# Kernel tuning notes

Measured on AMD Instinct MI355X. Metric: run time of the kernel, lower is better.

## Reference

```python
import jax, jax.numpy as jnp
import numpy as np
from jax import lax

N, C, RC, H, W = 2, 256, 32, 64, 64  # RC = C // 8


def conv1x1(x, w, b):
    # x: [n,c,h,w], w: [o,c], b: [o]
    return jnp.einsum('nchw,oc->nohw', x, w) + b[None, :, None, None]


def conv3x3(x, w, b):
    # x: [n,c,h,w], w: [o,i,3,3]
    y = lax.conv_general_dilated(x, w, window_strides=(1, 1), padding='SAME',
                                 dimension_numbers=('NCHW', 'OIHW', 'NCHW'))
    return y + b[None, :, None, None]


def setup_inputs() -> dict:
    key = jax.random.key(0)
    ks = jax.random.split(key, 16)
    p = lambda k, s: jax.random.normal(k, s, dtype=jnp.float32) * 0.02
    z = lambda o: jnp.zeros((o,), jnp.float32)
    return {
        'rgb_feat': jax.random.normal(ks[0], (N, C, H, W), jnp.float32),
        'chm_feat': jax.random.normal(ks[1], (N, C, H, W), jnp.float32),
        'rgb_q_w': p(ks[2], (RC, C)), 'rgb_q_b': z(RC),
        'rgb_k_w': p(ks[3], (RC, C)), 'rgb_k_b': z(RC),
        'rgb_v_w': p(ks[4], (C, C)), 'rgb_v_b': z(C),
        'depth_q_w': p(ks[5], (RC, C)), 'depth_q_b': z(RC),
        'depth_k_w': p(ks[6], (RC, C)), 'depth_k_b': z(RC),
        'depth_v_w': p(ks[7], (C, C)), 'depth_v_b': z(C),
        'gate_w': p(ks[8], (C, 2 * C)), 'gate_b': z(C),
        'fus1_w': p(ks[9], (2 * C, 2 * C)), 'fus1_b': z(2 * C),
        'fus2_w': p(ks[10], (2 * C, 2 * C, 3, 3)), 'fus2_b': z(2 * C),
        'fus3_w': p(ks[11], (C, 2 * C)), 'fus3_b': z(C),
        'skip_w': p(ks[12], (C, 2 * C)), 'skip_b': z(C),
    }


def reference(rgb_feat, chm_feat,
              rgb_q_w, rgb_q_b, rgb_k_w, rgb_k_b, rgb_v_w, rgb_v_b,
              depth_q_w, depth_q_b, depth_k_w, depth_k_b, depth_v_w, depth_v_b,
              gate_w, gate_b, fus1_w, fus1_b, fus2_w, fus2_b,
              fus3_w, fus3_b, skip_w, skip_b):
    n, c, h, w = rgb_feat.shape
    hw = h * w
    flat = lambda t: t.reshape(n, t.shape[1], hw)

    rq = flat(conv1x1(rgb_feat, rgb_q_w, rgb_q_b))       # [n,rc,hw]
    rk = flat(conv1x1(rgb_feat, rgb_k_w, rgb_k_b))       # [n,rc,hw]
    rv = flat(conv1x1(rgb_feat, rgb_v_w, rgb_v_b))       # [n,c,hw]
    dq = flat(conv1x1(chm_feat, depth_q_w, depth_q_b))   # [n,rc,hw]
    dk = flat(conv1x1(chm_feat, depth_k_w, depth_k_b))   # [n,rc,hw]
    dv = flat(conv1x1(chm_feat, depth_v_w, depth_v_b))   # [n,c,hw]

    # rgb branch attended with depth-derived attention
    rgb_attn = jax.nn.softmax(jnp.einsum('nri,nrj->nij', dq, dk), axis=-1)  # [n,hw,hw]
    br = jnp.einsum('nci,nij->ncj', rv, rgb_attn).reshape(rgb_feat.shape) + rgb_feat

    # depth branch attended with rgb-derived attention
    depth_attn = jax.nn.softmax(jnp.einsum('nri,nrj->nij', rq, rk), axis=-1)
    bd = jnp.einsum('nci,nij->ncj', dv, depth_attn).reshape(chm_feat.shape) + chm_feat

    cat = jnp.concatenate([br, bd], axis=1)              # [n,2c,h,w]
    g = jax.nn.sigmoid(conv1x1(cat, gate_w, gate_b))     # [n,c,h,w]
    c_fused = br * g + bd * (1.0 - g)
    d_fused = br * bd
    f = jnp.concatenate([c_fused, d_fused], axis=1)      # [n,2c,h,w]

    y = jax.nn.relu(conv1x1(f, fus1_w, fus1_b))
    y = jax.nn.relu(conv3x3(y, fus2_w, fus2_b))
    y = conv1x1(y, fus3_w, fus3_b)
    fused = y + conv1x1(f, skip_w, skip_b)
    return fused
```

## Files before the change

### kernel.cpp

```cpp
#include <hip/hip_runtime.h>
#include <stdint.h>


typedef __bf16 bf16_t;
typedef __bf16 bf16x8 __attribute__((ext_vector_type(8)));
typedef float f32x4 __attribute__((ext_vector_type(4)));

#define HW 4096
#define NB 2

__device__ inline f32x4 mfma_bf16(bf16x8 a, bf16x8 b, f32x4 c) {
    return __builtin_amdgcn_mfma_f32_16x16x32_bf16(a, b, c, 0, 0, 0);
}

#define LBAR()                                                                 \
    do {                                                                       \
        asm volatile("s_waitcnt lgkmcnt(0)" ::: "memory");                     \
        __builtin_amdgcn_s_barrier();                                          \
        __builtin_amdgcn_sched_barrier(0);                                     \
    } while (0)

#define MAXJOB 12
struct CvtJobs {
    const float* src[MAXJOB];
    bf16_t* dst[MAXJOB];
    int vend[MAXJOB];
    int rowlen[MAXJOB];
    int rowstride[MAXJOB];
    int rowoff[MAXJOB];
};

__global__ __launch_bounds__(256) void prep_k(CvtJobs J, int totalvec, int cvtBlocks,
                                              const float* __restrict__ fus2_src,
                                              bf16_t* __restrict__ fus2_dst,
                                              const float* qr, const float* kr,
                                              const float* qd, const float* kd,
                                              const float* sb, const float* fb,
                                              float* BQK_R, float* BQK_D, float* BSUM) {
    const int b = blockIdx.x, t = threadIdx.x;
    if (b < cvtBlocks) {
        int gv = b * 256 + t;
        if (gv >= totalvec) return;
        int j = 0;
        while (gv >= J.vend[j]) j++;
        int vbase = (j == 0) ? 0 : J.vend[j - 1];
        int e = (gv - vbase) * 8;
        const float* s = J.src[j] + e;
        float4 f0 = *(const float4*)s;
        float4 f1 = *(const float4*)(s + 4);
        bf16x8 o;
        o[0] = (bf16_t)f0.x; o[1] = (bf16_t)f0.y; o[2] = (bf16_t)f0.z; o[3] = (bf16_t)f0.w;
        o[4] = (bf16_t)f1.x; o[5] = (bf16_t)f1.y; o[6] = (bf16_t)f1.z; o[7] = (bf16_t)f1.w;
        int di = e;
        if (J.rowlen[j])
            di = (e / J.rowlen[j]) * J.rowstride[j] + J.rowoff[j] + (e % J.rowlen[j]);
        *(bf16x8*)(J.dst[j] + di) = o;
    } else if (b < cvtBlocks + 9216) {
        int idx = (b - cvtBlocks) * 256 + t;
        int o = idx / 4608;
        int tt = idx % 4608;
        int t9 = tt / 512;
        int c  = tt % 512;
        fus2_dst[idx] = (bf16_t)fus2_src[(size_t)o * 4608 + c * 9 + t9];
    } else {
        if (t < 32) {
            BQK_R[t] = qr[t]; BQK_R[32 + t] = kr[t];
            BQK_D[t] = qd[t]; BQK_D[32 + t] = kd[t];
        }
        BSUM[t] = sb[t] + fb[t];
    }
}

__global__ __launch_bounds__(512) void proj_k(const bf16_t* __restrict__ WV_R,
                                              const bf16_t* __restrict__ WV_D,
                                              const bf16_t* __restrict__ WQK_R,
                                              const bf16_t* __restrict__ WQK_D,
                                              const bf16_t* __restrict__ XB,
                                              const float* __restrict__ vb_r,
                                              const float* __restrict__ vb_d,
                                              const float* __restrict__ bqk_r,
                                              const float* __restrict__ bqk_d,
                                              bf16_t* __restrict__ V4,
                                              bf16_t* __restrict__ QKT) {
    __shared__ bf16_t Bt[2][64][72];
    const int t = threadIdx.x, b = blockIdx.x;
    const int w = t >> 6, lane = t & 63, quad = lane >> 4, l16 = lane & 15;

    f32x4 zero = {0.f, 0.f, 0.f, 0.f};
    f32x4 acc[4] = {zero, zero, zero, zero};

    if (b < 512) {
        const int mb = b & 1, jb = (b >> 1) & 63, n = b >> 7;
        const bf16_t* Au = (n >= 2) ? WV_D : WV_R;
        const float* biasu = (n >= 2) ? vb_d : vb_r;
        const bf16_t* Bb = XB + (size_t)n * (256 * HW) + jb * 64;
        const bf16_t* Arow = Au + (size_t)(mb * 128 + w * 16 + l16) * 256 + quad * 8;

        bf16x8 v0 = *(const bf16x8*)(Bb + (size_t)lane * HW + w * 8);
        for (int k0 = 0; k0 < 256; k0 += 64) {
            LBAR();
#pragma unroll
            for (int e = 0; e < 8; e++) Bt[0][w * 8 + e][lane] = v0[e];
            LBAR();
            const int kn = (k0 + 64 < 256) ? k0 + 64 : 0;
            bf16x8 vp = *(const bf16x8*)(Bb + (size_t)(kn + lane) * HW + w * 8);
            bf16x8 a0 = *(const bf16x8*)(Arow + k0);
            bf16x8 a1 = *(const bf16x8*)(Arow + k0 + 32);
#pragma unroll
            for (int ns = 0; ns < 4; ns++) {
                bf16x8 b0 = *(const bf16x8*)&Bt[0][ns * 16 + l16][quad * 8];
                bf16x8 b1 = *(const bf16x8*)&Bt[0][ns * 16 + l16][32 + quad * 8];
                acc[ns] = mfma_bf16(a0, b0, acc[ns]);
                acc[ns] = mfma_bf16(a1, b1, acc[ns]);
            }
            v0 = vp;
        }
#pragma unroll
        for (int ns = 0; ns < 4; ns++) {
#pragma unroll
            for (int rr = 0; rr < 4; rr++) {
                int m = mb * 128 + w * 16 + quad * 4 + rr;
                int col = jb * 64 + ns * 16 + l16;
                V4[(size_t)n * 256 * HW + (size_t)m * HW + col] =
                    (bf16_t)(acc[ns][rr] + biasu[m]);
            }
        }
    } else {
        const int qb = b - 512;
        const int n2 = qb >> 5, jpair = qb & 31;
        const int g = w >> 2, wg = w & 3;
        const int jb = jpair * 2 + g;
        const bf16_t* Au = (n2 >= 2) ? WQK_D : WQK_R;
        const float* biasu = (n2 >= 2) ? bqk_d : bqk_r;
        const bf16_t* Bb = XB + (size_t)n2 * (256 * HW) + jb * 64;
        const bf16_t* Arow = Au + (size_t)(wg * 16 + l16) * 256 + quad * 8;

        bf16x8 v0 = *(const bf16x8*)(Bb + (size_t)lane * HW + wg * 16);
        bf16x8 v1 = *(const bf16x8*)(Bb + (size_t)lane * HW + wg * 16 + 8);
        for (int k0 = 0; k0 < 256; k0 += 64) {
            LBAR();
#pragma unroll
            for (int e = 0; e < 8; e++) Bt[g][wg * 16 + e][lane] = v0[e];
#pragma unroll
            for (int e = 0; e < 8; e++) Bt[g][wg * 16 + 8 + e][lane] = v1[e];
            LBAR();
            const int kn = (k0 + 64 < 256) ? k0 + 64 : 0;
            bf16x8 p0 = *(const bf16x8*)(Bb + (size_t)(kn + lane) * HW + wg * 16);
            bf16x8 p1 = *(const bf16x8*)(Bb + (size_t)(kn + lane) * HW + wg * 16 + 8);
            bf16x8 a0 = *(const bf16x8*)(Arow + k0);
            bf16x8 a1 = *(const bf16x8*)(Arow + k0 + 32);
#pragma unroll
            for (int ns = 0; ns < 4; ns++) {
                bf16x8 b0 = *(const bf16x8*)&Bt[g][ns * 16 + l16][quad * 8];
                bf16x8 b1 = *(const bf16x8*)&Bt[g][ns * 16 + l16][32 + quad * 8];
                acc[ns] = mfma_bf16(a0, b0, acc[ns]);
                acc[ns] = mfma_bf16(a1, b1, acc[ns]);
            }
            v0 = p0; v1 = p1;
        }
        const float scl = (wg < 2) ? 1.44269504f : 1.0f;
#pragma unroll
        for (int ns = 0; ns < 4; ns++) {
            int col = jb * 64 + ns * 16 + l16;
            union { bf16_t h[4]; unsigned long long u; } pk;
#pragma unroll
            for (int rr = 0; rr < 4; rr++) {
                int m = wg * 16 + quad * 4 + rr;
                pk.h[rr] = (bf16_t)((acc[ns][rr] + biasu[m]) * scl);
            }
            *(unsigned long long*)(QKT +
                ((size_t)n2 * HW + col) * 64 + wg * 16 + quad * 4) = pk.u;
        }
    }
}

template <int EPI, bool OUT_BF16>
__global__ __launch_bounds__(512) void gemm_k(const bf16_t* __restrict__ A,
                                              const bf16_t* __restrict__ A2,
                                              const bf16_t* __restrict__ B,
                                              const float* __restrict__ bias,
                                              const float* __restrict__ bias2,
                                              void* __restrict__ outp,
                                              const void* __restrict__ aux,
                                              int M, int K, size_t strideB, size_t strideO) {
    __shared__ bf16_t Bt[64][72];
    const int t = threadIdx.x;
    const int mb = blockIdx.x, jb = blockIdx.y, n = blockIdx.z;
    const int w = t >> 6, lane = t & 63, quad = lane >> 4, l16 = lane & 15;

    const bf16_t* Au = (n >= 2) ? A2 : A;
    const float* biasu = (n >= 2) ? bias2 : bias;

    const bf16_t* Bb = B + (size_t)n * strideB + jb * 64;

    f32x4 zero = {0.f, 0.f, 0.f, 0.f};
    f32x4 acc[4] = {zero, zero, zero, zero};

    const bf16_t* Arow = Au + (size_t)(mb * 128 + w * 16 + l16) * K + quad * 8;

    bf16x8 v0 = *(const bf16x8*)(Bb + (size_t)lane * HW + w * 8);
    for (int k0 = 0; k0 < K; k0 += 64) {
        LBAR();
#pragma unroll
        for (int e = 0; e < 8; e++) Bt[w * 8 + e][lane] = v0[e];
        LBAR();
        const int kn = (k0 + 64 < K) ? k0 + 64 : 0;
        bf16x8 vp = *(const bf16x8*)(Bb + (size_t)(kn + lane) * HW + w * 8);
        bf16x8 a0 = *(const bf16x8*)(Arow + k0);
        bf16x8 a1 = *(const bf16x8*)(Arow + k0 + 32);
#pragma unroll
        for (int ns = 0; ns < 4; ns++) {
            bf16x8 b0 = *(const bf16x8*)&Bt[ns * 16 + l16][quad * 8];
            bf16x8 b1 = *(const bf16x8*)&Bt[ns * 16 + l16][32 + quad * 8];
            acc[ns] = mfma_bf16(a0, b0, acc[ns]);
            acc[ns] = mfma_bf16(a1, b1, acc[ns]);
        }
        v0 = vp;
    }

    if (EPI == 7) {
        const int m_base = mb * 128 + w * 16 + quad * 4;
#pragma unroll
        for (int ns = 0; ns < 4; ns++) {
            int col = jb * 64 + ns * 16 + l16;
            union { bf16_t h[4]; unsigned long long u; } pk;
#pragma unroll
            for (int rr = 0; rr < 4; rr++) {
                float v = acc[ns][rr] + biasu[m_base + rr];
                pk.h[rr] = (bf16_t)(v > 0.f ? v : 0.f);
            }
            *(unsigned long long*)((bf16_t*)outp +
                ((size_t)n * HW + col) * 512 + m_base) = pk.u;
        }
    } else if (EPI == 5) {
        const bf16_t* catp = (const bf16_t*)aux;
        bf16_t* f = (bf16_t*)outp;
#pragma unroll
        for (int ns = 0; ns < 4; ns++) {
#pragma unroll
            for (int rr = 0; rr < 4; rr++) {
                int m = mb * 128 + w * 16 + quad * 4 + rr;
                int col = jb * 64 + ns * 16 + l16;
                float v = acc[ns][rr] + biasu[m];
                float g = 1.f / (1.f + __expf(-v));
                size_t base = (size_t)n * 512 * HW + (size_t)m * HW + col;
                float br = (float)catp[base];
                float bd = (float)catp[base + (size_t)256 * HW];
                size_t ob = (size_t)n * 1024 * HW + (size_t)m * HW + col;
                f[ob] = (bf16_t)(br * g + bd * (1.f - g));
                f[ob + (size_t)256 * HW] = (bf16_t)(br * bd);
            }
        }
    } else {
#pragma unroll
        for (int ns = 0; ns < 4; ns++) {
#pragma unroll
            for (int rr = 0; rr < 4; rr++) {
                int m = mb * 128 + w * 16 + quad * 4 + rr;
                int col = jb * 64 + ns * 16 + l16;
                float v = acc[ns][rr] + biasu[m];
                size_t oi = (size_t)n * strideO + (size_t)m * HW + col;
                if (OUT_BF16) ((bf16_t*)outp)[oi] = (bf16_t)v;
                else ((float*)outp)[oi] = v;
            }
        }
    }
}

__global__ __launch_bounds__(256) void conv3_k(const bf16_t* __restrict__ A,
                                               const bf16_t* __restrict__ Y1n,
                                               const float* __restrict__ bias,
                                               bf16_t* __restrict__ outp,
                                               size_t strideN) {
    __shared__ bf16_t kTn[198][72];
    const int t = threadIdx.x;
    const int lin = blockIdx.x;
    const int n = lin & 1, mb = (lin >> 1) & 3, y = lin >> 3;
    const int w = t >> 6, lane = t & 63, quad = lane >> 4, l16 = lane & 15;

    f32x4 zero = {0.f, 0.f, 0.f, 0.f};
    f32x4 acc[2][4];
#pragma unroll
    for (int i = 0; i < 2; i++)
#pragma unroll
        for (int j = 0; j < 4; j++) acc[i][j] = zero;

    const bf16_t* Yb = Y1n + (size_t)n * HW * 512;

    const bf16_t* Arow0 = A + (size_t)(mb * 128 + w * 32 + l16) * 4608 + quad * 8;
    const bf16_t* Arow1 = Arow0 + (size_t)16 * 4608;

    int pxs[7], seg[7], gidx[7];
    bool ok[7], act[7];
#pragma unroll
    for (int i = 0; i < 7; i++) {
        int slot = t + i * 256;
        act[i] = slot < 1584;
        int ps = act[i] ? (slot >> 3) : 0;
        pxs[i] = ps;
        seg[i] = slot & 7;
        int r = ps / 66, xm = ps % 66;
        int yy = y + r - 1, xx = xm - 1;
        ok[i] = act[i] && ((unsigned)yy < 64u) && ((unsigned)xx < 64u);
        gidx[i] = ok[i] ? (yy * 64 + xx) : 0;
    }

    bf16x8 vals[7];
#pragma unroll
    for (int i = 0; i < 7; i++) {
        bf16x8 v;
        if (ok[i]) {
            v = *(const bf16x8*)(Yb + (size_t)gidx[i] * 512 + seg[i] * 8);
        } else {
#pragma unroll
            for (int e = 0; e < 8; e++) v[e] = (bf16_t)0.f;
        }
        vals[i] = v;
    }

    for (int c0 = 0; c0 < 512; c0 += 64) {
        LBAR();
#pragma unroll
        for (int i = 0; i < 7; i++)
            if (act[i]) *(bf16x8*)&kTn[pxs[i]][seg[i] * 8] = vals[i];
        LBAR();

        const int cn = (c0 + 64) & 511;
#pragma unroll
        for (int i = 0; i < 7; i++) {
            bf16x8 v;
            if (ok[i]) {
                v = *(const bf16x8*)(Yb + (size_t)gidx[i] * 512 + cn + seg[i] * 8);
            } else {
#pragma unroll
                for (int e = 0; e < 8; e++) v[e] = (bf16_t)0.f;
            }
            vals[i] = v;
        }

#pragma unroll
        for (int t9 = 0; t9 < 9; t9++) {
            const int dy = t9 / 3, dx = t9 % 3;
            const bf16_t* ap0 = Arow0 + t9 * 512 + c0;
            const bf16_t* ap1 = Arow1 + t9 * 512 + c0;
            bf16x8 a00 = *(const bf16x8*)(ap0);
            bf16x8 a01 = *(const bf16x8*)(ap0 + 32);
            bf16x8 a10 = *(const bf16x8*)(ap1);
            bf16x8 a11 = *(const bf16x8*)(ap1 + 32);
#pragma unroll
            for (int ns = 0; ns < 4; ns++) {
                int p = dy * 66 + ns * 16 + l16 + dx;
                bf16x8 b0 = *(const bf16x8*)&kTn[p][quad * 8];
                bf16x8 b1 = *(const bf16x8*)&kTn[p][32 + quad * 8];
                acc[0][ns] = mfma_bf16(a00, b0, acc[0][ns]);
                acc[0][ns] = mfma_bf16(a01, b1, acc[0][ns]);
                acc[1][ns] = mfma_bf16(a10, b0, acc[1][ns]);
                acc[1][ns] = mfma_bf16(a11, b1, acc[1][ns]);
            }
        }
    }

#pragma unroll
    for (int ms = 0; ms < 2; ms++) {
#pragma unroll
        for (int ns = 0; ns < 4; ns++) {
#pragma unroll
            for (int rr = 0; rr < 4; rr++) {
                int m = mb * 128 + w * 32 + ms * 16 + quad * 4 + rr;
                int x = ns * 16 + l16;
                float v = acc[ms][ns][rr] + bias[m];
                v = v > 0.f ? v : 0.f;
                outp[(size_t)n * strideN + (size_t)m * HW + y * 64 + x] = (bf16_t)v;
            }
        }
    }
}

#define ASTEP(P, ASC, AVC, ASN, AVN, ITN)                                      \
    {                                                                          \
        _Pragma("unroll")                                                      \
        for (int ns = 0; ns < 4; ns++) {                                       \
            f32x4 s = mfma_bf16(ASC, bS[ns], zero);                            \
            union { bf16_t h[4]; unsigned long long u; } pk;                   \
            float zs = 0.f;                                                    \
            _Pragma("unroll")                                                  \
            for (int rr = 0; rr < 4; rr++) {                                   \
                pk.h[rr] = (bf16_t)__builtin_amdgcn_exp2f(s[rr]);              \
                zs += (float)pk.h[rr];                                         \
            }                                                                  \
            zacc[ns] += zs;                                                    \
            *(unsigned long long*)&PT[P][ns * 16 + l16][w * 16 + quad * 4] = pk.u; \
        }                                                                      \
        ASN = *(const bf16x8*)(Qa + (size_t)((ITN) & 63) * (64 * 64));         \
        AVN[0][0] = *(const bf16x8*)(Vr0 + ((ITN) & 63) * 64);                 \
        AVN[0][1] = *(const bf16x8*)(Vr0 + ((ITN) & 63) * 64 + 32);            \
        AVN[1][0] = *(const bf16x8*)(Vr1 + ((ITN) & 63) * 64);                 \
        AVN[1][1] = *(const bf16x8*)(Vr1 + ((ITN) & 63) * 64 + 32);            \
        asm volatile("s_waitcnt lgkmcnt(0)" ::: "memory");                     \
        __builtin_amdgcn_s_barrier();                                          \
        __builtin_amdgcn_sched_barrier(0);                                     \
        __builtin_amdgcn_s_setprio(1);                                         \
        _Pragma("unroll")                                                      \
        for (int ns = 0; ns < 4; ns++) {                                       \
            bf16x8 b0 = *(const bf16x8*)&PT[P][ns * 16 + l16][quad * 8];       \
            bf16x8 b1 = *(const bf16x8*)&PT[P][ns * 16 + l16][32 + quad * 8];  \
            _Pragma("unroll")                                                  \
            for (int ct = 0; ct < 2; ct++) {                                   \
                acc[ct][ns] = mfma_bf16(AVC[ct][0], b0, acc[ct][ns]);          \
                acc[ct][ns] = mfma_bf16(AVC[ct][1], b1, acc[ct][ns]);          \
            }                                                                  \
        }                                                                      \
        __builtin_amdgcn_s_setprio(0);                                         \
    }

__global__ __launch_bounds__(256) void attn3_k(const bf16_t* __restrict__ QKT,
                                               const bf16_t* __restrict__ V,
                                               const float* __restrict__ rgb_feat,
                                               const float* __restrict__ chm_feat,
                                               bf16_t* __restrict__ CAT) {
    __shared__ bf16_t PT[2][64][72];
    __shared__ float Zp[4][64];
    const int t = threadIdx.x;
    const int lin = blockIdx.x;
    const int cb = lin & 1, z = (lin >> 1) & 3, jb = lin >> 3;
    const int w = t >> 6, lane = t & 63, quad = lane >> 4, l16 = lane & 15;
    const int qs = z ^ 2, n = z & 1;

    const bf16_t* Q = QKT + (size_t)qs * HW * 64;

    bf16x8 bS[4];
#pragma unroll
    for (int ns = 0; ns < 4; ns++)
        bS[ns] = *(const bf16x8*)(Q + (size_t)(jb * 64 + ns * 16 + l16) * 64 + 32 + quad * 8);

    f32x4 zero = {0.f, 0.f, 0.f, 0.f};
    f32x4 acc[2][4];
#pragma unroll
    for (int i = 0; i < 2; i++)
#pragma unroll
        for (int j = 0; j < 4; j++) acc[i][j] = zero;
    float zacc[4] = {0.f, 0.f, 0.f, 0.f};

    const bf16_t* Vr0 = V + ((size_t)z * 256 + cb * 128 + w * 16 + l16) * HW + quad * 8;
    const bf16_t* Vr1 = Vr0 + (size_t)64 * HW;
    const bf16_t* Qa = Q + (size_t)(w * 16 + l16) * 64 + quad * 8;

    bf16x8 aSa, aSb, aVa[2][2], aVb[2][2];
    aSa = *(const bf16x8*)Qa;
    aVa[0][0] = *(const bf16x8*)(Vr0);
    aVa[0][1] = *(const bf16x8*)(Vr0 + 32);
    aVa[1][0] = *(const bf16x8*)(Vr1);
    aVa[1][1] = *(const bf16x8*)(Vr1 + 32);

    for (int ii = 0; ii < 32; ii++) {
        ASTEP(0, aSa, aVa, aSb, aVb, 2 * ii + 1);
        ASTEP(1, aSb, aVb, aSa, aVa, 2 * ii + 2);
    }

#pragma unroll
    for (int ns = 0; ns < 4; ns++) {
        zacc[ns] += __shfl_xor(zacc[ns], 16, 64);
        zacc[ns] += __shfl_xor(zacc[ns], 32, 64);
    }
    if (lane < 16) {
#pragma unroll
        for (int ns = 0; ns < 4; ns++) Zp[w][ns * 16 + lane] = zacc[ns];
    }
    __syncthreads();
    float rz[4];
#pragma unroll
    for (int ns = 0; ns < 4; ns++) {
        float ssum = 0.f;
#pragma unroll
        for (int ww = 0; ww < 4; ww++) ssum += Zp[ww][ns * 16 + l16];
        rz[ns] = 1.f / ssum;
    }

    const float* feat = ((z < 2) ? rgb_feat : chm_feat) + (size_t)n * 256 * HW;
    bf16_t* outp = CAT + (size_t)n * 512 * HW + (size_t)(z < 2 ? 0 : 256) * HW;
#pragma unroll
    for (int ct = 0; ct < 2; ct++) {
#pragma unroll
        for (int ns = 0; ns < 4; ns++) {
#pragma unroll
            for (int rr = 0; rr < 4; rr++) {
                int c = cb * 128 + ct * 64 + w * 16 + quad * 4 + rr;
                int col = jb * 64 + ns * 16 + l16;
                float v = acc[ct][ns][rr] * rz[ns] + feat[(size_t)c * HW + col];
                outp[(size_t)c * HW + col] = (bf16_t)v;
            }
        }
    }
}

extern "C" void kernel_launch(void* const* d_in, const int* in_sizes, int n_in,
                              void* d_out, int out_size, void* d_ws, size_t ws_size,
                              hipStream_t stream) {
    (void)in_sizes; (void)n_in; (void)out_size; (void)ws_size;

    const float* rgb_feat  = (const float*)d_in[0];
    const float* chm_feat  = (const float*)d_in[1];
    const float* rgb_q_w   = (const float*)d_in[2];
    const float* rgb_q_b   = (const float*)d_in[3];
    const float* rgb_k_w   = (const float*)d_in[4];
    const float* rgb_k_b   = (const float*)d_in[5];
    const float* rgb_v_w   = (const float*)d_in[6];
    const float* rgb_v_b   = (const float*)d_in[7];
    const float* depth_q_w = (const float*)d_in[8];
    const float* depth_q_b = (const float*)d_in[9];
    const float* depth_k_w = (const float*)d_in[10];
    const float* depth_k_b = (const float*)d_in[11];
    const float* depth_v_w = (const float*)d_in[12];
    const float* depth_v_b = (const float*)d_in[13];
    const float* gate_w    = (const float*)d_in[14];
    const float* gate_b    = (const float*)d_in[15];
    const float* fus1_w    = (const float*)d_in[16];
    const float* fus1_b    = (const float*)d_in[17];
    const float* fus2_w    = (const float*)d_in[18];
    const float* fus2_b    = (const float*)d_in[19];
    const float* fus3_w    = (const float*)d_in[20];
    const float* fus3_b    = (const float*)d_in[21];
    const float* skip_w    = (const float*)d_in[22];
    const float* skip_b    = (const float*)d_in[23];

    char* ws = (char*)d_ws;
    size_t off = 0;
    auto alloc = [&](size_t bytes) -> char* {
        char* p = ws + off;
        off += (bytes + 255) & ~(size_t)255;
        return p;
    };

    bf16_t* WQK_R = (bf16_t*)alloc(64 * 256 * 2);
    bf16_t* WQK_D = (bf16_t*)alloc(64 * 256 * 2);
    bf16_t* WV_R  = (bf16_t*)alloc(256 * 256 * 2);
    bf16_t* WV_D  = (bf16_t*)alloc(256 * 256 * 2);
    bf16_t* WGATE = (bf16_t*)alloc(256 * 512 * 2);
    bf16_t* WFUS1 = (bf16_t*)alloc(512 * 512 * 2);
    bf16_t* WFUS2 = (bf16_t*)alloc(512 * 4608 * 2);
    bf16_t* WCAT  = (bf16_t*)alloc(256 * 1024 * 2);
    float*  BQK_R = (float*)alloc(64 * 4);
    float*  BQK_D = (float*)alloc(64 * 4);
    float*  BSUM  = (float*)alloc(256 * 4);
    bf16_t* XB    = (bf16_t*)alloc((size_t)4 * 256 * HW * 2);
    bf16_t* QKT   = (bf16_t*)alloc((size_t)4 * HW * 64 * 2);
    bf16_t* V4    = (bf16_t*)alloc((size_t)4 * 256 * HW * 2);
    bf16_t* CAT   = (bf16_t*)alloc((size_t)NB * 512 * HW * 2);
    bf16_t* FY    = (bf16_t*)alloc((size_t)NB * 1024 * HW * 2);
    bf16_t* Y1    = (bf16_t*)alloc((size_t)NB * HW * 512 * 2);

    bf16_t* XR = XB;
    bf16_t* XC = XB + (size_t)2 * 256 * HW;

    CvtJobs J;
    int cum = 0, nj = 0;
    auto addjob = [&](const float* s, bf16_t* d, int cnt, int rl, int rs, int ro) {
        J.src[nj] = s; J.dst[nj] = d; cum += cnt / 8; J.vend[nj] = cum;
        J.rowlen[nj] = rl; J.rowstride[nj] = rs; J.rowoff[nj] = ro; nj++;
    };
    addjob(rgb_feat, XR, NB * 256 * HW, 0, 0, 0);
    addjob(chm_feat, XC, NB * 256 * HW, 0, 0, 0);
    addjob(rgb_q_w, WQK_R, 32 * 256, 0, 0, 0);
    addjob(rgb_k_w, WQK_R + 32 * 256, 32 * 256, 0, 0, 0);
    addjob(depth_q_w, WQK_D, 32 * 256, 0, 0, 0);
    addjob(depth_k_w, WQK_D + 32 * 256, 32 * 256, 0, 0, 0);
    addjob(rgb_v_w, WV_R, 256 * 256, 0, 0, 0);
    addjob(depth_v_w, WV_D, 256 * 256, 0, 0, 0);
    addjob(gate_w, WGATE, 256 * 512, 0, 0, 0);
    addjob(fus1_w, WFUS1, 512 * 512, 0, 0, 0);
    addjob(skip_w, WCAT, 256 * 512, 512, 1024, 0);
    addjob(fus3_w, WCAT, 256 * 512, 512, 1024, 512);
    int totalvec = cum;
    int cvtBlocks = (totalvec + 255) / 256;
    int prepBlocks = cvtBlocks + 9216 + 1;
    prep_k<<<dim3(prepBlocks), 256, 0, stream>>>(
        J, totalvec, cvtBlocks, fus2_w, WFUS2,
        rgb_q_b, rgb_k_b, depth_q_b, depth_k_b, skip_b, fus3_b,
        BQK_R, BQK_D, BSUM);

    proj_k<<<dim3(640), 512, 0, stream>>>(
        WV_R, WV_D, WQK_R, WQK_D, XB, rgb_v_b, depth_v_b, BQK_R, BQK_D, V4, QKT);

    attn3_k<<<dim3(512), 256, 0, stream>>>(QKT, V4, rgb_feat, chm_feat, CAT);

    gemm_k<5, true><<<dim3(2, 64, NB), 512, 0, stream>>>(
        WGATE, WGATE, CAT, gate_b, gate_b, FY, CAT, 256, 512, (size_t)512 * HW, 0);

    gemm_k<7, true><<<dim3(4, 64, NB), 512, 0, stream>>>(
        WFUS1, WFUS1, FY, fus1_b, fus1_b, Y1, nullptr, 512, 512, (size_t)1024 * HW, 0);

    conv3_k<<<dim3(512), 256, 0, stream>>>(WFUS2, Y1, fus2_b,
                                           FY + (size_t)512 * HW, (size_t)1024 * HW);

    gemm_k<0, false><<<dim3(2, 64, NB), 512, 0, stream>>>(
        WCAT, WCAT, FY, BSUM, BSUM, d_out, nullptr, 256, 1024, (size_t)1024 * HW, (size_t)256 * HW);
}
```

Measured before the change: 335.6 us.

## Warp-specialize attention into producer softmax and consumer PV waves

Splits the attention kernel into 4 producer waves that compute exp scores into shared memory and 4 consumer waves that run the P·V MFMAs, synchronized by alternating barriers on a double-buffered PT tile. Each block now covers all 256 channels for one column tile, so the score computation is no longer repeated across two channel-half blocks. Grid halves and block size doubles to 512 threads. This adds register pressure (16 accumulators per consumer wave) and tight barrier coupling between the two roles.

```diff
diff --git a/kernel.cpp b/kernel.cpp
--- a/kernel.cpp
+++ b/kernel.cpp
@@ -376,7 +376,7 @@
     }
 }
 
-#define ASTEP(P, ASC, AVC, ASN, AVN, ITN)                                      \
+#define PSTEP(P, ASC, ASN, ITN)                                                \
     {                                                                          \
         _Pragma("unroll")                                                      \
         for (int ns = 0; ns < 4; ns++) {                                       \
@@ -392,11 +392,13 @@
             *(unsigned long long*)&PT[P][ns * 16 + l16][w * 16 + quad * 4] = pk.u; \
         }                                                                      \
         ASN = *(const bf16x8*)(Qa + (size_t)((ITN) & 63) * (64 * 64));         \
-        AVN[0][0] = *(const bf16x8*)(Vr0 + ((ITN) & 63) * 64);                 \
-        AVN[0][1] = *(const bf16x8*)(Vr0 + ((ITN) & 63) * 64 + 32);            \
-        AVN[1][0] = *(const bf16x8*)(Vr1 + ((ITN) & 63) * 64);                 \
-        AVN[1][1] = *(const bf16x8*)(Vr1 + ((ITN) & 63) * 64 + 32);            \
         asm volatile("s_waitcnt lgkmcnt(0)" ::: "memory");                     \
+        __builtin_amdgcn_s_barrier();                                          \
+        __builtin_amdgcn_sched_barrier(0);                                     \
+    }
+
+#define CSTEP(P, AVC, AVN, ITN)                                                \
+    {                                                                          \
         __builtin_amdgcn_s_barrier();                                          \
         __builtin_amdgcn_sched_barrier(0);                                     \
         __builtin_amdgcn_s_setprio(1);                                         \
@@ -405,15 +407,22 @@
             bf16x8 b0 = *(const bf16x8*)&PT[P][ns * 16 + l16][quad * 8];       \
             bf16x8 b1 = *(const bf16x8*)&PT[P][ns * 16 + l16][32 + quad * 8];  \
             _Pragma("unroll")                                                  \
-            for (int ct = 0; ct < 2; ct++) {                                   \
+            for (int ct = 0; ct < 4; ct++) {                                   \
                 acc[ct][ns] = mfma_bf16(AVC[ct][0], b0, acc[ct][ns]);          \
                 acc[ct][ns] = mfma_bf16(AVC[ct][1], b1, acc[ct][ns]);          \
             }                                                                  \
         }                                                                      \
         __builtin_amdgcn_s_setprio(0);                                         \
-    }
-
-__global__ __launch_bounds__(256) void attn3_k(const bf16_t* __restrict__ QKT,
+        _Pragma("unroll")                                                      \
+        for (int ct = 0; ct < 4; ct++) {                                       \
+            AVN[ct][0] = *(const bf16x8*)(Vr[ct] + ((ITN) & 63) * 64);         \
+            AVN[ct][1] = *(const bf16x8*)(Vr[ct] + ((ITN) & 63) * 64 + 32);    \
+        }                                                                      \
+        asm volatile("s_waitcnt lgkmcnt(0)" ::: "memory");                     \
+        __builtin_amdgcn_sched_barrier(0);                                     \
+    }
+
+__global__ __launch_bounds__(512) void attn3_k(const bf16_t* __restrict__ QKT,
                                                const bf16_t* __restrict__ V,
                                                const float* __restrict__ rgb_feat,
                                                const float* __restrict__ chm_feat,
@@ -422,72 +431,89 @@
     __shared__ float Zp[4][64];
     const int t = threadIdx.x;
     const int lin = blockIdx.x;
-    const int cb = lin & 1, z = (lin >> 1) & 3, jb = lin >> 3;
+    const int z = (lin >> 1) & 3;
+    const int jb = ((lin >> 3) << 1) | (lin & 1);
     const int w = t >> 6, lane = t & 63, quad = lane >> 4, l16 = lane & 15;
     const int qs = z ^ 2, n = z & 1;
 
     const bf16_t* Q = QKT + (size_t)qs * HW * 64;
-
-    bf16x8 bS[4];
-#pragma unroll
-    for (int ns = 0; ns < 4; ns++)
-        bS[ns] = *(const bf16x8*)(Q + (size_t)(jb * 64 + ns * 16 + l16) * 64 + 32 + quad * 8);
-
     f32x4 zero = {0.f, 0.f, 0.f, 0.f};
-    f32x4 acc[2][4];
-#pragma unroll
-    for (int i = 0; i < 2; i++)
-#pragma unroll
-        for (int j = 0; j < 4; j++) acc[i][j] = zero;
-    float zacc[4] = {0.f, 0.f, 0.f, 0.f};
-
-    const bf16_t* Vr0 = V + ((size_t)z * 256 + cb * 128 + w * 16 + l16) * HW + quad * 8;
-    const bf16_t* Vr1 = Vr0 + (size_t)64 * HW;
-    const bf16_t* Qa = Q + (size_t)(w * 16 + l16) * 64 + quad * 8;
-
-    bf16x8 aSa, aSb, aVa[2][2], aVb[2][2];
-    aSa = *(const bf16x8*)Qa;
-    aVa[0][0] = *(const bf16x8*)(Vr0);
-    aVa[0][1] = *(const bf16x8*)(Vr0 + 32);
-    aVa[1][0] = *(const bf16x8*)(Vr1);
-    aVa[1][1] = *(const bf16x8*)(Vr1 + 32);
-
-    for (int ii = 0; ii < 32; ii++) {
-        ASTEP(0, aSa, aVa, aSb, aVb, 2 * ii + 1);
-        ASTEP(1, aSb, aVb, aSa, aVa, 2 * ii + 2);
-    }
-
-#pragma unroll
-    for (int ns = 0; ns < 4; ns++) {
-        zacc[ns] += __shfl_xor(zacc[ns], 16, 64);
-        zacc[ns] += __shfl_xor(zacc[ns], 32, 64);
-    }
-    if (lane < 16) {
-#pragma unroll
-        for (int ns = 0; ns < 4; ns++) Zp[w][ns * 16 + lane] = zacc[ns];
-    }
-    __syncthreads();
-    float rz[4];
-#pragma unroll
-    for (int ns = 0; ns < 4; ns++) {
-        float ssum = 0.f;
-#pragma unroll
-        for (int ww = 0; ww < 4; ww++) ssum += Zp[ww][ns * 16 + l16];
-        rz[ns] = 1.f / ssum;
-    }
-
-    const float* feat = ((z < 2) ? rgb_feat : chm_feat) + (size_t)n * 256 * HW;
-    bf16_t* outp = CAT + (size_t)n * 512 * HW + (size_t)(z < 2 ? 0 : 256) * HW;
-#pragma unroll
-    for (int ct = 0; ct < 2; ct++) {
-#pragma unroll
-        for (int ns = 0; ns < 4; ns++) {
-#pragma unroll
-            for (int rr = 0; rr < 4; rr++) {
-                int c = cb * 128 + ct * 64 + w * 16 + quad * 4 + rr;
-                int col = jb * 64 + ns * 16 + l16;
-                float v = acc[ct][ns][rr] * rz[ns] + feat[(size_t)c * HW + col];
-                outp[(size_t)c * HW + col] = (bf16_t)v;
+
+    if (w < 4) {
+        bf16x8 bS[4];
+#pragma unroll
+        for (int ns = 0; ns < 4; ns++)
+            bS[ns] = *(const bf16x8*)(Q + (size_t)(jb * 64 + ns * 16 + l16) * 64 + 32 + quad * 8);
+        float zacc[4] = {0.f, 0.f, 0.f, 0.f};
+        const bf16_t* Qa = Q + (size_t)(w * 16 + l16) * 64 + quad * 8;
+
+        bf16x8 aSa, aSb;
+        aSa = *(const bf16x8*)Qa;
+
+        for (int ii = 0; ii < 32; ii++) {
+            PSTEP(0, aSa, aSb, 2 * ii + 1);
+            PSTEP(1, aSb, aSa, 2 * ii + 2);
+        }
+
+#pragma unroll
+        for (int ns = 0; ns < 4; ns++) {
+            zacc[ns] += __shfl_xor(zacc[ns], 16, 64);
+            zacc[ns] += __shfl_xor(zacc[ns], 32, 64);
+        }
+        if (lane < 16) {
+#pragma unroll
+            for (int ns = 0; ns < 4; ns++) Zp[w][ns * 16 + lane] = zacc[ns];
+        }
+        __syncthreads();
+    } else {
+        const int wc = w - 4;
+        f32x4 acc[4][4];
+#pragma unroll
+        for (int i = 0; i < 4; i++)
+#pragma unroll
+            for (int j = 0; j < 4; j++) acc[i][j] = zero;
+
+        const bf16_t* Vr[4];
+#pragma unroll
+        for (int ct = 0; ct < 4; ct++)
+            Vr[ct] = V + ((size_t)z * 256 + wc * 64 + ct * 16 + l16) * HW + quad * 8;
+
+        bf16x8 aVa[4][2], aVb[4][2];
+#pragma unroll
+        for (int ct = 0; ct < 4; ct++) {
+            aVa[ct][0] = *(const bf16x8*)(Vr[ct]);
+            aVa[ct][1] = *(const bf16x8*)(Vr[ct] + 32);
+        }
+
+        for (int ii = 0; ii < 32; ii++) {
+            CSTEP(0, aVa, aVb, 2 * ii + 1);
+            CSTEP(1, aVb, aVa, 2 * ii + 2);
+        }
+
+        __syncthreads();
+
+        float rz[4];
+#pragma unroll
+        for (int ns = 0; ns < 4; ns++) {
+            float ssum = 0.f;
+#pragma unroll
+            for (int ww = 0; ww < 4; ww++) ssum += Zp[ww][ns * 16 + l16];
+            rz[ns] = 1.f / ssum;
+        }
+
+        const float* feat = ((z < 2) ? rgb_feat : chm_feat) + (size_t)n * 256 * HW;
+        bf16_t* outp = CAT + (size_t)n * 512 * HW + (size_t)(z < 2 ? 0 : 256) * HW;
+#pragma unroll
+        for (int ct = 0; ct < 4; ct++) {
+#pragma unroll
+            for (int ns = 0; ns < 4; ns++) {
+#pragma unroll
+                for (int rr = 0; rr < 4; rr++) {
+                    int c = wc * 64 + ct * 16 + quad * 4 + rr;
+                    int col = jb * 64 + ns * 16 + l16;
+                    float v = acc[ct][ns][rr] * rz[ns] + feat[(size_t)c * HW + col];
+                    outp[(size_t)c * HW + col] = (bf16_t)v;
+                }
             }
         }
     }
@@ -581,7 +607,7 @@
     proj_k<<<dim3(640), 512, 0, stream>>>(
         WV_R, WV_D, WQK_R, WQK_D, XB, rgb_v_b, depth_v_b, BQK_R, BQK_D, V4, QKT);
 
-    attn3_k<<<dim3(512), 256, 0, stream>>>(QKT, V4, rgb_feat, chm_feat, CAT);
+    attn3_k<<<dim3(256), 512, 0, stream>>>(QKT, V4, rgb_feat, chm_feat, CAT);
 
     gemm_k<5, true><<<dim3(2, 64, NB), 512, 0, stream>>>(
         WGATE, WGATE, CAT, gate_b, gate_b, FY, CAT, 256, 512, (size_t)512 * HW, 0);
```

Result: faster. 328.6 us (median of 2 runs) (-2.1%).
